# Kernel optimization log

Measured on AMD Instinct MI355X. Metric: run time of the kernel, lower is better.

## Reference

```python
import jax, jax.numpy as jnp
import numpy as np

LAM = 0.3          # margin weight lam (halved inside, as in the torch code)
IGNORE = 255       # ignore_index
NEG = -1e30        # finite -inf stand-in for masking the label class


def setup_inputs() -> dict:
    key = jax.random.key(0)
    k1, k2 = jax.random.split(key)
    logits = jax.random.normal(k1, (8, 19, 512, 512), dtype=jnp.float32)
    labels = jax.random.randint(k2, (8, 512, 512), 0, 19)  # no ignored pixels
    return {"logits": logits, "labels": labels}


def _loss_per_pixel(logits, lb):
    # logits: (N, C, H, W) float32, lb: (N, H, W) int in [0, C)
    C = logits.shape[1]
    coeff = 1.0 / (C - 1.0)
    lam = LAM / 2.0
    onehot = jax.nn.one_hot(lb, C, axis=1, dtype=jnp.bool_)  # (N, C, H, W)
    # softmax over the C-1 non-label classes == softmax with label class masked out
    m_logits = jnp.where(onehot, NEG, logits)
    log_q = jax.nn.log_softmax(m_logits, axis=1)
    q = jnp.exp(log_q)
    margin = jnp.where(onehot, 0.0, (q - coeff) * log_q).sum(axis=1) * lam  # (N, H, W)
    # standard cross-entropy term: -log_softmax(logits)[label]
    log_p = jax.nn.log_softmax(logits, axis=1)
    ce = -jnp.take_along_axis(log_p, lb[:, None], axis=1)[:, 0]  # (N, H, W)
    return margin + ce


def reference(logits, labels):
    valid = labels != IGNORE
    lb = jnp.where(valid, labels, 0)
    loss = _loss_per_pixel(logits.astype(jnp.float32), lb)
    vf = valid.astype(loss.dtype)
    # reduction='mean' over non-ignored pixels
    return (loss * vf).sum() / vf.sum()
```

## Files before the change

kernel.cpp:

```cpp
#include <hip/hip_runtime.h>

#define NCLS 19
#define HW (512 * 512)
#define NPIX (8 * HW)

__device__ __forceinline__ float fexp(float x) { return __expf(x); }
__device__ __forceinline__ float flog(float x) { return __logf(x); }

__global__ __launch_bounds__(256) void lms_main_kernel(
    const float* __restrict__ logits, const int* __restrict__ labels,
    float* __restrict__ ws) {
  const float COEFF = 1.0f / 18.0f;
  const float LAM_HALF = 0.15f;

  int t = blockIdx.x * blockDim.x + threadIdx.x;
  long p = (long)t * 4;

  float loss = 0.0f;
  float cnt = 0.0f;

  if (p < NPIX) {
    int n = (int)(p / HW);
    int hw = (int)(p % HW);
    const float* base = logits + (size_t)n * NCLS * HW + hw;

    int4 lb4 = *(const int4*)(labels + p);
    int lbs[4] = {lb4.x, lb4.y, lb4.z, lb4.w};

    float4 x[NCLS];
#pragma unroll
    for (int c = 0; c < NCLS; ++c)
      x[c] = *(const float4*)(base + (size_t)c * HW);

#pragma unroll
    for (int j = 0; j < 4; ++j) {
      float xv[NCLS];
#pragma unroll
      for (int c = 0; c < NCLS; ++c) xv[c] = ((const float*)&x[c])[j];

      int lb = lbs[j];
      bool valid = (lb != 255);
      int l = valid ? lb : 0;

      float M = xv[0];
#pragma unroll
      for (int c = 1; c < NCLS; ++c) M = fmaxf(M, xv[c]);

      float s_all = 0.0f;
#pragma unroll
      for (int c = 0; c < NCLS; ++c) s_all += fexp(xv[c] - M);
      float x_l = xv[l];
      float e_l = fexp(x_l - M);
      float s_m = s_all - e_l;

      float lse = M + flog(s_all);
      float lse_m = M + flog(s_m);
      float inv_sm = 1.0f / s_m;

      float msum = 0.0f;
#pragma unroll
      for (int c = 0; c < NCLS; ++c) {
        float e = fexp(xv[c] - M);
        float term = (e * inv_sm - COEFF) * (xv[c] - lse_m);
        msum += (c == l) ? 0.0f : term;
      }

      float ce = lse - x_l;
      float pixel_loss = ce + LAM_HALF * msum;
      loss += valid ? pixel_loss : 0.0f;
      cnt += valid ? 1.0f : 0.0f;
    }
  }

#pragma unroll
  for (int off = 32; off > 0; off >>= 1) {
    loss += __shfl_down(loss, off, 64);
    cnt += __shfl_down(cnt, off, 64);
  }

  __shared__ float sl[4], sc[4];
  int wave = threadIdx.x >> 6;
  int lane = threadIdx.x & 63;
  if (lane == 0) {
    sl[wave] = loss;
    sc[wave] = cnt;
  }
  __syncthreads();
  if (threadIdx.x == 0) {
    float L = sl[0] + sl[1] + sl[2] + sl[3];
    float Cn = sc[0] + sc[1] + sc[2] + sc[3];
    atomicAdd(ws, L);
    atomicAdd(ws + 1, Cn);
  }
}

__global__ void lms_final_kernel(const float* __restrict__ ws,
                                 float* __restrict__ out) {
  out[0] = ws[0] / ws[1];
}

extern "C" void kernel_launch(void* const* d_in, const int* in_sizes, int n_in,
                              void* d_out, int out_size, void* d_ws, size_t ws_size,
                              hipStream_t stream) {
  const float* logits = (const float*)d_in[0];
  const int* labels = (const int*)d_in[1];
  float* out = (float*)d_out;
  float* ws = (float*)d_ws;

  hipMemsetAsync(ws, 0, 2 * sizeof(float), stream);

  int threads = 256;
  int quads = NPIX / 4;
  int blocks = (quads + threads - 1) / threads;
  lms_main_kernel<<<blocks, threads, 0, stream>>>(logits, labels, ws);
  lms_final_kernel<<<1, 1, 0, stream>>>(ws, out);
}
```

Measured before the change: 237.8 us.

## Simplify margin term algebraically to single exp pass and halve pixels per thread

Rewrites the margin sum using the identity that the log-sum-exp terms cancel, so it only needs the accumulated sums of exp·x, exp and x. This removes a second loop of exponentials and a log per pixel. Each thread also processes two pixels with float2 loads instead of four, reducing register pressure. Computing the masked sums by subtraction can lose precision when the label class dominates.

```diff
diff --git a/kernel.cpp b/kernel.cpp
--- a/kernel.cpp
+++ b/kernel.cpp
@@ -3,9 +3,6 @@
 #define NCLS 19
 #define HW (512 * 512)
 #define NPIX (8 * HW)
-
-__device__ __forceinline__ float fexp(float x) { return __expf(x); }
-__device__ __forceinline__ float flog(float x) { return __logf(x); }
 
 __global__ __launch_bounds__(256) void lms_main_kernel(
     const float* __restrict__ logits, const int* __restrict__ labels,
@@ -14,7 +11,7 @@
   const float LAM_HALF = 0.15f;
 
   int t = blockIdx.x * blockDim.x + threadIdx.x;
-  long p = (long)t * 4;
+  long p = (long)t * 2;
 
   float loss = 0.0f;
   float cnt = 0.0f;
@@ -24,49 +21,49 @@
     int hw = (int)(p % HW);
     const float* base = logits + (size_t)n * NCLS * HW + hw;
 
-    int4 lb4 = *(const int4*)(labels + p);
-    int lbs[4] = {lb4.x, lb4.y, lb4.z, lb4.w};
+    int2 lb2 = *(const int2*)(labels + p);
 
-    float4 x[NCLS];
+    float2 x[NCLS];
 #pragma unroll
     for (int c = 0; c < NCLS; ++c)
-      x[c] = *(const float4*)(base + (size_t)c * HW);
+      x[c] = *(const float2*)(base + (size_t)c * HW);
 
 #pragma unroll
-    for (int j = 0; j < 4; ++j) {
-      float xv[NCLS];
-#pragma unroll
-      for (int c = 0; c < NCLS; ++c) xv[c] = ((const float*)&x[c])[j];
-
-      int lb = lbs[j];
+    for (int j = 0; j < 2; ++j) {
+      int lb = j ? lb2.y : lb2.x;
       bool valid = (lb != 255);
       int l = valid ? lb : 0;
 
-      float M = xv[0];
+      float M = j ? x[0].y : x[0].x;
 #pragma unroll
-      for (int c = 1; c < NCLS; ++c) M = fmaxf(M, xv[c]);
+      for (int c = 1; c < NCLS; ++c) {
+        float xv = j ? x[c].y : x[c].x;
+        M = fmaxf(M, xv);
+      }
 
       float s_all = 0.0f;
-#pragma unroll
-      for (int c = 0; c < NCLS; ++c) s_all += fexp(xv[c] - M);
-      float x_l = xv[l];
-      float e_l = fexp(x_l - M);
-      float s_m = s_all - e_l;
-
-      float lse = M + flog(s_all);
-      float lse_m = M + flog(s_m);
-      float inv_sm = 1.0f / s_m;
-
-      float msum = 0.0f;
+      float T = 0.0f;
+      float S = 0.0f;
+      float x_l = 0.0f;
 #pragma unroll
       for (int c = 0; c < NCLS; ++c) {
-        float e = fexp(xv[c] - M);
-        float term = (e * inv_sm - COEFF) * (xv[c] - lse_m);
-        msum += (c == l) ? 0.0f : term;
+        float xv = j ? x[c].y : x[c].x;
+        float e = __expf(xv - M);
+        s_all += e;
+        T += e * xv;
+        S += xv;
+        x_l = (c == l) ? xv : x_l;
       }
 
-      float ce = lse - x_l;
-      float pixel_loss = ce + LAM_HALF * msum;
+      float e_l = __expf(x_l - M);
+      float s_m = s_all - e_l;
+      float T_m = T - e_l * x_l;
+      float S_m = S - x_l;
+
+      float margin = T_m / s_m - COEFF * S_m;
+      float ce = M + __logf(s_all) - x_l;
+
+      float pixel_loss = ce + LAM_HALF * margin;
       loss += valid ? pixel_loss : 0.0f;
       cnt += valid ? 1.0f : 0.0f;
     }
@@ -87,10 +84,8 @@
   }
   __syncthreads();
   if (threadIdx.x == 0) {
-    float L = sl[0] + sl[1] + sl[2] + sl[3];
-    float Cn = sc[0] + sc[1] + sc[2] + sc[3];
-    atomicAdd(ws, L);
-    atomicAdd(ws + 1, Cn);
+    atomicAdd(ws, sl[0] + sl[1] + sl[2] + sl[3]);
+    atomicAdd(ws + 1, sc[0] + sc[1] + sc[2] + sc[3]);
   }
 }
 
@@ -110,8 +105,8 @@
   hipMemsetAsync(ws, 0, 2 * sizeof(float), stream);
 
   int threads = 256;
-  int quads = NPIX / 4;
-  int blocks = (quads + threads - 1) / threads;
+  int pairs = NPIX / 2;
+  int blocks = (pairs + threads - 1) / threads;
   lms_main_kernel<<<blocks, threads, 0, stream>>>(logits, labels, ws);
   lms_final_kernel<<<1, 1, 0, stream>>>(ws, out);
 }
```

Result: slower. 282.3 us (+18.7%).
